# Performance work log

Measured on AMD Instinct MI355X. Metric: run time of the kernel, lower is better.

## Reference

```python
import jax, jax.numpy as jnp
import numpy as np

BATCH = 4096
DIM = 128
TEMP = 0.5

def setup_inputs() -> dict:
    key = jax.random.key(0)
    k1, k2 = jax.random.split(key)
    proj_1 = jax.random.normal(k1, (BATCH, DIM), dtype=jnp.float32)
    proj_2 = jax.random.normal(k2, (BATCH, DIM), dtype=jnp.float32)
    return {"proj_1": proj_1, "proj_2": proj_2}

def _l2norm(x, eps=1e-12):
    # matches F.normalize(p=2, dim=1)
    n = jnp.sqrt(jnp.sum(x * x, axis=1, keepdims=True))
    return x / jnp.maximum(n, eps)

def reference(proj_1, proj_2):
    B = proj_1.shape[0]
    z_i = _l2norm(proj_1)
    z_j = _l2norm(proj_2)
    reps = jnp.concatenate([z_i, z_j], axis=0)          # [2B, D]
    # cosine similarity of normalized vectors == dot product; (2B,D)x(D,2B) matmul
    sim = reps @ reps.T                                 # [2B, 2B]
    sim_ij = jnp.einsum('bd,bd->b', z_i, z_j)           # diag(sim, +B)
    sim_ji = sim_ij                                     # diag(sim, -B) is symmetric
    positives = jnp.concatenate([sim_ij, sim_ji], axis=0)  # [2B]
    nominator = jnp.exp(positives / TEMP)
    mask = (~jnp.eye(2 * B, dtype=bool)).astype(sim.dtype)
    denominator = jnp.sum(mask * jnp.exp(sim / TEMP), axis=1)  # [2B]
    all_losses = -jnp.log(nominator / denominator)
    loss = jnp.sum(all_losses) / (2 * B)
    return loss
```

## Files before the change

kernel.cpp:

```cpp
#include <hip/hip_runtime.h>
#include <hip/hip_bf16.h>
#include <math.h>

#define BATCH 4096
#define DIM 128
#define TWO_B 8192
#define SCALE 1.69864374f

typedef float floatx4 __attribute__((ext_vector_type(4)));
typedef int   intx4  __attribute__((ext_vector_type(4)));
typedef long  longx2 __attribute__((ext_vector_type(2)));

__device__ __forceinline__ longx2 as_l2(intx4 v) {
    union { intx4 a; longx2 b; } u; u.a = v; return u.b;
}
__device__ __forceinline__ unsigned char to_fp8(float v) {
    return (unsigned char)(__builtin_amdgcn_cvt_pk_fp8_f32(v, v, 0, false) & 0xff);
}


__global__ __launch_bounds__(256) void norm_kernel(const float* __restrict__ p1,
                                                   const float* __restrict__ p2,
                                                   unsigned char* __restrict__ repsF,
                                                   float* __restrict__ pos,
                                                   float* __restrict__ out) {
    int tid = threadIdx.x;
    int w = tid >> 6, l = tid & 63;
    int b = blockIdx.x * 4 + w;
    const float* r1 = p1 + (size_t)b * DIM;
    const float* r2 = p2 + (size_t)b * DIM;
    float x0 = r1[l], x1 = r1[l + 64];
    float y0 = r2[l], y1 = r2[l + 64];
    float s1 = x0 * x0 + x1 * x1;
    float s2 = y0 * y0 + y1 * y1;
    float s12 = x0 * y0 + x1 * y1;
    #pragma unroll
    for (int off = 32; off; off >>= 1) {
        s1  += __shfl_xor(s1, off);
        s2  += __shfl_xor(s2, off);
        s12 += __shfl_xor(s12, off);
    }
    float n1 = fmaxf(sqrtf(s1), 1e-12f);
    float n2 = fmaxf(sqrtf(s2), 1e-12f);
    float i1 = SCALE / n1;
    float i2 = SCALE / n2;

    int r1i = b, r2i = b + BATCH;
    int off0 = ((l >> 5) & 1) * 8 + ((l >> 3) & 3) * 256 + (l & 7);
    size_t a1 = (size_t)(r1i >> 4) * 2048 + (r1i & 15) * 16 + off0;
    size_t a2 = (size_t)(r2i >> 4) * 2048 + (r2i & 15) * 16 + off0;
    repsF[a1]        = to_fp8(x0 * i1);
    repsF[a1 + 1024] = to_fp8(x1 * i1);
    repsF[a2]        = to_fp8(y0 * i2);
    repsF[a2 + 1024] = to_fp8(y1 * i2);

    if (l == 0) {
        pos[b] = s12 / (n1 * n2);
        if (b == 0) out[0] = 0.0f;
    }
}

__global__ __launch_bounds__(256, 4) void sim_kernel(const unsigned char* __restrict__ repsF,
                                                     float* __restrict__ part) {
    __shared__ float lds[4][16][68];
    int tid = threadIdx.x;
    int wid = tid >> 6, lane = tid & 63;
    int wm = wid >> 1, wn = wid & 1;
    int lr = lane & 15, q = lane >> 4;
    int r = blockIdx.y;
    int c = blockIdx.x;
    int TM, TN;
    if (c < 64 - r) { TM = r;      TN = r + c; }
    else            { TM = 63 - r; TN = TM + (c - (64 - r)); }
    if (TM == TN && wm == 1 && wn == 0) return;
    int tm = 2 * TM + wm, tn = 2 * TN + wn;
    bool diag = (tm == tn);

    const char* base = (const char*)repsF;
    int lofs = q * 256 + lr * 16;
    const char* ab = base + tm * 8192 + lofs;
    const char* bb = base + tn * 8192 + lofs;

    longx2 aF[4][2], bF[4][2];
    #pragma unroll
    for (int mi = 0; mi < 4; ++mi)
        #pragma unroll
        for (int h = 0; h < 2; ++h) {
            aF[mi][h] = as_l2(*(const intx4*)(ab + mi * 2048 + h * 1024));
            bF[mi][h] = as_l2(*(const intx4*)(bb + mi * 2048 + h * 1024));
        }

    float cs[4] = {0.0f, 0.0f, 0.0f, 0.0f};
    floatx4 rpacc[4];

    #pragma unroll
    for (int p = 0; p < 2; ++p) {
        floatx4 acc[4][2] = {};
        #pragma unroll
        for (int ck = 0; ck < 4; ++ck) {
            int h = ck >> 1, sel = ck & 1;
            #pragma unroll
            for (int mi = 0; mi < 4; ++mi)
                #pragma unroll
                for (int nn = 0; nn < 2; ++nn)
                    acc[mi][nn] = __builtin_amdgcn_mfma_f32_16x16x32_fp8_fp8(
                        aF[mi][h][sel], bF[2 * p + nn][h][sel], acc[mi][nn], 0, 0, 0);
        }
        #pragma unroll
        for (int mi = 0; mi < 4; ++mi) {
            #pragma unroll
            for (int reg = 0; reg < 4; ++reg) {
                float e0 = __builtin_amdgcn_exp2f(acc[mi][0][reg]);
                float e1 = __builtin_amdgcn_exp2f(acc[mi][1][reg]);
                if (diag && (q * 4 + reg) == lr) {
                    if (mi == 2 * p)     e0 = 0.0f;
                    if (mi == 2 * p + 1) e1 = 0.0f;
                }
                cs[2 * p]     += e0;
                cs[2 * p + 1] += e1;
                float rsum = e0 + e1;
                rpacc[mi][reg] = (p == 0) ? rsum : (rpacc[mi][reg] + rsum);
            }
        }
    }

    float* myl = &lds[wid][0][0];
    #pragma unroll
    for (int mi = 0; mi < 4; ++mi)
        *(floatx4*)&myl[lr * 68 + mi * 16 + q * 4] = rpacc[mi];
    asm volatile("s_waitcnt lgkmcnt(0)" ::: "memory");
    {
        float rs = 0.0f;
        #pragma unroll
        for (int j = 0; j < 16; ++j)
            rs += myl[j * 68 + lane];
        part[(size_t)tn * TWO_B + tm * 64 + lane] = rs;
    }
    if (!diag) {
        #pragma unroll
        for (int ni = 0; ni < 4; ++ni) {
            cs[ni] += __shfl_xor(cs[ni], 16);
            cs[ni] += __shfl_xor(cs[ni], 32);
        }
        if (q == 0) {
            #pragma unroll
            for (int ni = 0; ni < 4; ++ni)
                part[(size_t)tm * TWO_B + tn * 64 + ni * 16 + lr] = cs[ni];
        }
    }
}

__global__ __launch_bounds__(256) void reduce_kernel(const float* __restrict__ part,
                                                     const float* __restrict__ pos,
                                                     float* __restrict__ out) {
    __shared__ float stage[4][64];
    int tid = threadIdx.x;
    int w = tid >> 6, l = tid & 63;
    int rr = blockIdx.x * 64 + l;
    const float* p = part + (size_t)(w * 32) * TWO_B + rr;
    float s0 = 0.0f, s1 = 0.0f, s2 = 0.0f, s3 = 0.0f;
    #pragma unroll
    for (int k = 0; k < 32; k += 4) {
        s0 += p[(size_t)(k + 0) * TWO_B];
        s1 += p[(size_t)(k + 1) * TWO_B];
        s2 += p[(size_t)(k + 2) * TWO_B];
        s3 += p[(size_t)(k + 3) * TWO_B];
    }
    stage[w][l] = (s0 + s1) + (s2 + s3);
    __syncthreads();
    if (w == 0) {
        float s = (stage[0][l] + stage[1][l]) + (stage[2][l] + stage[3][l]);
        float v = __logf(s) - 2.0f * pos[rr & (BATCH - 1)];
        #pragma unroll
        for (int off = 32; off; off >>= 1) v += __shfl_xor(v, off);
        if (l == 0) atomicAdd(out, v * (1.0f / TWO_B));
    }
}

extern "C" void kernel_launch(void* const* d_in, const int* in_sizes, int n_in,
                              void* d_out, int out_size, void* d_ws, size_t ws_size,
                              hipStream_t stream) {
    const float* p1 = (const float*)d_in[0];
    const float* p2 = (const float*)d_in[1];
    float* out = (float*)d_out;

    char* ws = (char*)d_ws;
    unsigned char* repsF = (unsigned char*)ws;
    float* pos  = (float*)(ws + (size_t)TWO_B * DIM);
    float* part = pos + BATCH;

    norm_kernel<<<BATCH / 4, 256, 0, stream>>>(p1, p2, repsF, pos, out);
    sim_kernel<<<dim3(65, 32), 256, 0, stream>>>(repsF, part);
    reduce_kernel<<<TWO_B / 64, 256, 0, stream>>>(part, pos, out);
}
```

Before: 73.57 us.

## Accumulate row denominators with atomics instead of partial buffer reduction

The sim kernel now adds its per-row and per-column exp sums straight into an 8192-entry denominator array with float atomics, where before it wrote them into a large 128x8192 partial buffer. This removes that buffer's write traffic and the strided read-back in the reduce kernel, which is replaced by a light finish kernel. The norm kernel zeroes the denominator array. The cost is atomic contention on shared addresses (about 128 adds per entry) and a summation order that is no longer fixed, so results can vary slightly between runs.

```diff
diff --git a/kernel.cpp b/kernel.cpp
--- a/kernel.cpp
+++ b/kernel.cpp
@@ -23,8 +23,10 @@
                                                    const float* __restrict__ p2,
                                                    unsigned char* __restrict__ repsF,
                                                    float* __restrict__ pos,
+                                                   float* __restrict__ denom,
                                                    float* __restrict__ out) {
     int tid = threadIdx.x;
+    if (tid < 8) denom[blockIdx.x * 8 + tid] = 0.0f;
     int w = tid >> 6, l = tid & 63;
     int b = blockIdx.x * 4 + w;
     const float* r1 = p1 + (size_t)b * DIM;
@@ -61,7 +63,7 @@
 }
 
 __global__ __launch_bounds__(256, 4) void sim_kernel(const unsigned char* __restrict__ repsF,
-                                                     float* __restrict__ part) {
+                                                     float* __restrict__ denom) {
     __shared__ float lds[4][16][68];
     int tid = threadIdx.x;
     int wid = tid >> 6, lane = tid & 63;
@@ -134,7 +136,7 @@
         #pragma unroll
         for (int j = 0; j < 16; ++j)
             rs += myl[j * 68 + lane];
-        part[(size_t)tn * TWO_B + tm * 64 + lane] = rs;
+        atomicAdd(&denom[tm * 64 + lane], rs);
     }
     if (!diag) {
         #pragma unroll
@@ -145,36 +147,19 @@
         if (q == 0) {
             #pragma unroll
             for (int ni = 0; ni < 4; ++ni)
-                part[(size_t)tm * TWO_B + tn * 64 + ni * 16 + lr] = cs[ni];
+                atomicAdd(&denom[tn * 64 + ni * 16 + lr], cs[ni]);
         }
     }
 }
 
-__global__ __launch_bounds__(256) void reduce_kernel(const float* __restrict__ part,
+__global__ __launch_bounds__(256) void finish_kernel(const float* __restrict__ denom,
                                                      const float* __restrict__ pos,
                                                      float* __restrict__ out) {
-    __shared__ float stage[4][64];
-    int tid = threadIdx.x;
-    int w = tid >> 6, l = tid & 63;
-    int rr = blockIdx.x * 64 + l;
-    const float* p = part + (size_t)(w * 32) * TWO_B + rr;
-    float s0 = 0.0f, s1 = 0.0f, s2 = 0.0f, s3 = 0.0f;
+    int r = blockIdx.x * 256 + threadIdx.x;
+    float v = __logf(denom[r]) - 2.0f * pos[r & (BATCH - 1)];
     #pragma unroll
-    for (int k = 0; k < 32; k += 4) {
-        s0 += p[(size_t)(k + 0) * TWO_B];
-        s1 += p[(size_t)(k + 1) * TWO_B];
-        s2 += p[(size_t)(k + 2) * TWO_B];
-        s3 += p[(size_t)(k + 3) * TWO_B];
-    }
-    stage[w][l] = (s0 + s1) + (s2 + s3);
-    __syncthreads();
-    if (w == 0) {
-        float s = (stage[0][l] + stage[1][l]) + (stage[2][l] + stage[3][l]);
-        float v = __logf(s) - 2.0f * pos[rr & (BATCH - 1)];
-        #pragma unroll
-        for (int off = 32; off; off >>= 1) v += __shfl_xor(v, off);
-        if (l == 0) atomicAdd(out, v * (1.0f / TWO_B));
-    }
+    for (int off = 32; off; off >>= 1) v += __shfl_xor(v, off);
+    if ((threadIdx.x & 63) == 0) atomicAdd(out, v * (1.0f / TWO_B));
 }
 
 extern "C" void kernel_launch(void* const* d_in, const int* in_sizes, int n_in,
@@ -186,10 +171,10 @@
 
     char* ws = (char*)d_ws;
     unsigned char* repsF = (unsigned char*)ws;
-    float* pos  = (float*)(ws + (size_t)TWO_B * DIM);
-    float* part = pos + BATCH;
+    float* pos   = (float*)(ws + (size_t)TWO_B * DIM);
+    float* denom = pos + BATCH;
 
-    norm_kernel<<<BATCH / 4, 256, 0, stream>>>(p1, p2, repsF, pos, out);
-    sim_kernel<<<dim3(65, 32), 256, 0, stream>>>(repsF, part);
-    reduce_kernel<<<TWO_B / 64, 256, 0, stream>>>(part, pos, out);
+    norm_kernel<<<BATCH / 4, 256, 0, stream>>>(p1, p2, repsF, pos, denom, out);
+    sim_kernel<<<dim3(65, 32), 256, 0, stream>>>(repsF, denom);
+    finish_kernel<<<TWO_B / 256, 256, 0, stream>>>(denom, pos, out);
 }
```

After: 74.27 us. About the same (+1.0%).
